# Kernel optimization log

Hardware: AMD Instinct MI355X
Metric: run time of the kernel (lower is better)

## Reference

```python
import jax, jax.numpy as jnp
import numpy as np

B, T, C = 2, 2048, 2048
N_HEAD, N_KV = 16, 4
HD = C // N_HEAD          # 128
ROPE_THETA = 10000.0


def setup_inputs() -> dict:
    key = jax.random.key(0)
    ks = jax.random.split(key, 6)
    std = 0.02
    x = jax.random.normal(ks[0], (B, T, C), dtype=jnp.float32)
    Wq = jax.random.normal(ks[1], (C, C), dtype=jnp.float32) * std
    Wk = jax.random.normal(ks[2], (C, N_KV * HD), dtype=jnp.float32) * std
    Wv = jax.random.normal(ks[3], (C, N_KV * HD), dtype=jnp.float32) * std
    Wo = jax.random.normal(ks[4], (C, C), dtype=jnp.float32) * std
    # real RoPE frequencies: freqs_cis = exp(i * t * theta^{-2j/hd})
    inv_freq = 1.0 / (ROPE_THETA ** (jnp.arange(0, HD, 2, dtype=jnp.float32) / HD))
    ang = jnp.arange(T, dtype=jnp.float32)[:, None] * inv_freq[None, :]  # [T, HD//2]
    return {"x": x, "Wq": Wq, "Wk": Wk, "Wv": Wv, "Wo": Wo,
            "freqs_cos": jnp.cos(ang), "freqs_sin": jnp.sin(ang)}


def _rope(t, cos, sin):
    # t: [B, H, T, HD]; cos/sin: [T, HD//2] -> complex rotate even/odd pairs
    tr = t.reshape(*t.shape[:-1], HD // 2, 2)
    re, im = tr[..., 0], tr[..., 1]
    c = cos[None, None, :, :]
    s = sin[None, None, :, :]
    out = jnp.stack([re * c - im * s, re * s + im * c], axis=-1)
    return out.reshape(t.shape)


def reference(x, Wq, Wk, Wv, Wo, freqs_cos, freqs_sin):
    Bm, Tm, Cm = x.shape
    q = (x @ Wq).reshape(Bm, Tm, N_HEAD, HD).transpose(0, 2, 1, 3)  # [B,H,T,HD]
    k = (x @ Wk).reshape(Bm, Tm, N_KV, HD).transpose(0, 2, 1, 3)    # [B,Hkv,T,HD]
    v = (x @ Wv).reshape(Bm, Tm, N_KV, HD).transpose(0, 2, 1, 3)
    q = _rope(q, freqs_cos, freqs_sin)
    k = _rope(k, freqs_cos, freqs_sin)
    rep = N_HEAD // N_KV
    k = jnp.repeat(k, rep, axis=1)  # GQA repeat_kv -> [B,H,T,HD]
    v = jnp.repeat(v, rep, axis=1)
    scale = 1.0 / jnp.sqrt(jnp.asarray(HD, dtype=x.dtype))
    att = jnp.einsum("bhqd,bhkd->bhqk", q, k) * scale
    causal = jnp.tril(jnp.ones((Tm, Tm), dtype=bool))
    att = jnp.where(causal[None, None], att, jnp.asarray(-jnp.inf, att.dtype))
    att = jax.nn.softmax(att, axis=-1)
    y = jnp.einsum("bhqk,bhkd->bhqd", att, v)
    y = y.transpose(0, 2, 1, 3).reshape(Bm, Tm, Cm)
    return y @ Wo
```

## Files before the change

### kernel.cpp

```cpp
#include <hip/hip_runtime.h>

#define B_ 2
#define T_ 2048
#define C_ 2048
#define NH_ 16
#define NKV_ 4
#define HD_ 128
#define REP_ (NH_ / NKV_)
#define LDQKV 3072

typedef unsigned short u16;
typedef __bf16 bf16x8v __attribute__((ext_vector_type(8)));
typedef float f32x4v __attribute__((ext_vector_type(4)));

__device__ __forceinline__ u16 f2bf(float f) {
    unsigned int u;
    __builtin_memcpy(&u, &f, 4);
    u += 0x7FFFu + ((u >> 16) & 1u);
    return (u16)(u >> 16);
}
__device__ __forceinline__ unsigned int cvtpk(float a, float b) {
    unsigned int r;
    asm("v_cvt_pk_bf16_f32 %0, %1, %2" : "=v"(r) : "v"(a), "v"(b));
    return r;
}
__device__ __forceinline__ bf16x8v load8(const u16* p) {
    return *reinterpret_cast<const bf16x8v*>(p);
}
__device__ __forceinline__ void gl16(const u16* g, u16* l) {
    __builtin_amdgcn_global_load_lds(
        (const __attribute__((address_space(1))) void*)(g),
        (__attribute__((address_space(3))) void*)(l), 16, 0, 0);
}
__device__ __forceinline__ void stg(const u16* g, u16* l, int tid, int K) {
    gl16(g, l + tid * 8);
    gl16(g + (size_t)64 * K, l + 4096 + tid * 8);
}
__device__ __forceinline__ void stgB3(const u16* g, u16* l, int tid, int K) {
    gl16(g, l + tid * 8);
    gl16(g + (size_t)64 * K, l + 4096 + tid * 8);
    gl16(g + (size_t)128 * K, l + 8192 + tid * 8);
}
#define BAR()      __builtin_amdgcn_s_barrier()
#define LGKM0()    asm volatile("s_waitcnt lgkmcnt(0)" ::: "memory")
#define SCHED0()   __builtin_amdgcn_sched_barrier(0)
#define PRIO(x)    __builtin_amdgcn_s_setprio(x)

__global__ void cvt_f32_bf16(const float* __restrict__ in, u16* __restrict__ out, int n4) {
    int i = blockIdx.x * blockDim.x + threadIdx.x;
    if (i >= n4) return;
    float4 v = reinterpret_cast<const float4*>(in)[i];
    ushort4 o;
    o.x = f2bf(v.x); o.y = f2bf(v.y); o.z = f2bf(v.z); o.w = f2bf(v.w);
    reinterpret_cast<ushort4*>(out)[i] = o;
}

__global__ void xpose_f32_bf16(const float* __restrict__ in, u16* __restrict__ out,
                               int R, int Cc) {
    __shared__ u16 tile[32][33];
    int bx = blockIdx.x * 32, by = blockIdx.y * 32;
    int tx = threadIdx.x, ty = threadIdx.y;
    for (int i = 0; i < 32; i += 8)
        tile[ty + i][tx] = f2bf(in[(size_t)(by + ty + i) * Cc + bx + tx]);
    __syncthreads();
    for (int i = 0; i < 32; i += 8)
        out[(size_t)(bx + ty + i) * R + by + tx] = tile[tx][ty + i];
}

__global__ __launch_bounds__(512, 2) void gemm_qkv(const u16* __restrict__ A,
                                                   const u16* __restrict__ BT,
                                                   u16* __restrict__ Cq,
                                                   u16* __restrict__ vtb,
                                                   const float* __restrict__ cb,
                                                   const float* __restrict__ sb,
                                                   int M, int N, int K) {
    __shared__ __align__(16) u16 As[2][2][8192];
    __shared__ __align__(16) u16 Bs[2][12288];
    int tid = threadIdx.x;
    int lane = tid & 63, wave = tid >> 6;
    int wm = wave >> 2, wn = wave & 3;
    int m15 = lane & 15, quad = lane >> 4;

    int nbx = N / 192;
    int bid = blockIdx.x, cpx = gridDim.x >> 3;
    int swz = (bid & 7) * cpx + (bid >> 3);
    int m0 = (swz / nbx) * 256, n0 = (swz % nbx) * 192;

    int r_ = tid >> 3, c_ = tid & 7;
    const u16* gA0 = A + (size_t)(m0 + r_) * K + ((c_ ^ (r_ & 7)) * 8);
    const u16* gB0 = BT + (size_t)(n0 + r_) * K + ((c_ ^ (r_ & 7)) * 8);

    int sw8 = m15 & 7;
    int co0 = (quad ^ sw8) * 8;
    int co1 = ((4 + quad) ^ sw8) * 8;
    const u16* aB = &As[0][0][0] + wm * 8192 + m15 * 64;
    const u16* bB = &Bs[0][0] + (wn * 48 + m15) * 64;

    f32x4v acc[8][3] = {};
    int NT = K >> 6;

    stgB3(gB0, &Bs[0][0], tid, K);
    stg(gA0, &As[0][0][0], tid, K);
    stg(gA0 + (size_t)128 * K, &As[0][1][0], tid, K);
    stgB3(gB0 + 64, &Bs[1][0], tid, K);
    asm volatile("s_waitcnt vmcnt(3)" ::: "memory");
    SCHED0();
    BAR();

    for (int t = 0; t < NT; t++) {
        int d = t & 1;
        const u16* aT = aB + d * 16384;
        const u16* bT = bB + d * 12288;
        bf16x8v a0[4][2], a1[4][2], bv[3][2];

#pragma unroll
        for (int mt = 0; mt < 4; mt++) {
            a0[mt][0] = load8(aT + mt * 1024 + co0);
            a0[mt][1] = load8(aT + mt * 1024 + co1);
        }
#pragma unroll
        for (int nt = 0; nt < 2; nt++) {
            bv[nt][0] = load8(bT + nt * 1024 + co0);
            bv[nt][1] = load8(bT + nt * 1024 + co1);
        }
        if (t + 1 < NT) stg(gA0 + (t + 1) * 64, &As[1 - d][0][0], tid, K);
        BAR(); LGKM0(); SCHED0(); PRIO(1);
#pragma unroll
        for (int kc = 0; kc < 2; kc++)
#pragma unroll
            for (int mt = 0; mt < 4; mt++)
#pragma unroll
                for (int nt = 0; nt < 2; nt++)
                    acc[mt][nt] = __builtin_amdgcn_mfma_f32_16x16x32_bf16(
                        a0[mt][kc], bv[nt][kc], acc[mt][nt], 0, 0, 0);
        PRIO(0); BAR();

#pragma unroll
        for (int mt = 0; mt < 4; mt++) {
            a1[mt][0] = load8(aT + (mt + 4) * 1024 + co0);
            a1[mt][1] = load8(aT + (mt + 4) * 1024 + co1);
        }
        bv[2][0] = load8(bT + 2048 + co0);
        bv[2][1] = load8(bT + 2048 + co1);
        if (t + 1 < NT) stg(gA0 + (size_t)128 * K + (t + 1) * 64, &As[1 - d][1][0], tid, K);
        BAR(); LGKM0(); SCHED0(); PRIO(1);
#pragma unroll
        for (int kc = 0; kc < 2; kc++)
#pragma unroll
            for (int mt = 0; mt < 4; mt++)
#pragma unroll
                for (int nt = 0; nt < 2; nt++)
                    acc[mt + 4][nt] = __builtin_amdgcn_mfma_f32_16x16x32_bf16(
                        a1[mt][kc], bv[nt][kc], acc[mt + 4][nt], 0, 0, 0);
        PRIO(0); BAR();

        if (t + 2 < NT) stgB3(gB0 + (t + 2) * 64, &Bs[d][0], tid, K);
        PRIO(1);
#pragma unroll
        for (int kc = 0; kc < 2; kc++)
#pragma unroll
            for (int mt = 0; mt < 4; mt++)
                acc[mt][2] = __builtin_amdgcn_mfma_f32_16x16x32_bf16(
                    a0[mt][kc], bv[2][kc], acc[mt][2], 0, 0, 0);
#pragma unroll
        for (int kc = 0; kc < 2; kc++)
#pragma unroll
            for (int mt = 0; mt < 4; mt++)
                acc[mt + 4][2] = __builtin_amdgcn_mfma_f32_16x16x32_bf16(
                    a1[mt][kc], bv[2][kc], acc[mt + 4][2], 0, 0, 0);
        PRIO(0);
        if (t + 2 < NT) { asm volatile("s_waitcnt vmcnt(3)" ::: "memory"); }
        else            { asm volatile("s_waitcnt vmcnt(0)" ::: "memory"); }
        SCHED0();
        BAR();
    }

#pragma unroll
    for (int mt = 0; mt < 8; mt++)
#pragma unroll
        for (int nt = 0; nt < 3; nt++) {
            int c = n0 + wn * 48 + nt * 16 + m15;
            if (c >= 2560) {
                int hd = c - 2560;
                int mbase = m0 + wm * 128 + mt * 16 + quad * 4;
                int bb = mbase >> 11, tok = mbase & 2047;
                int g = (tok & 31) >> 2;
                int off = (tok & ~31) + ((g & 3) * 8 + (g >> 2) * 4);
                ushort4 pk;
                pk.x = f2bf(acc[mt][nt][0]);
                pk.y = f2bf(acc[mt][nt][1]);
                pk.z = f2bf(acc[mt][nt][2]);
                pk.w = f2bf(acc[mt][nt][3]);
                *reinterpret_cast<ushort4*>(vtb + ((size_t)bb * 512 + hd) * T_ + off) = pk;
            } else {
                int i = (c & 127) >> 1;
                float sgn = (c & 1) ? 1.f : -1.f;
#pragma unroll
                for (int r = 0; r < 4; r++) {
                    int mrow = m0 + wm * 128 + mt * 16 + quad * 4 + r;
                    int tok = mrow & 2047;
                    float cv = cb[tok * 64 + i];
                    float sv = sb[tok * 64 + i];
                    float v = acc[mt][nt][r];
                    float pval = __shfl_xor(v, 1, 64);
                    float outv = fmaf(v, cv, pval * sv * sgn);
                    Cq[(size_t)mrow * N + c] = f2bf(outv);
                }
            }
        }
}

__global__ __launch_bounds__(512, 2) void gemm_out(const u16* __restrict__ A,
                                                   const u16* __restrict__ BT,
                                                   float* __restrict__ C,
                                                   int M, int N, int K) {
    __shared__ __align__(16) u16 As2[2][8192];
    __shared__ __align__(16) u16 Bs2[2][2][8192];
    int tid = threadIdx.x;
    int lane = tid & 63, wave = tid >> 6;
    int wm = wave >> 2, wn = wave & 3;
    int m15 = lane & 15, quad = lane >> 4;

    int nbx = N >> 8;
    int bid = blockIdx.x, cpx = gridDim.x >> 3;
    int swz = (bid & 7) * cpx + (bid >> 3);
    int m0 = (swz / nbx) * 128, n0 = (swz % nbx) * 256;

    const u16* gA0 = A + (size_t)(m0 + (tid >> 3)) * K + (((tid & 7) ^ ((tid >> 3) & 7)) * 8);
    const u16* gB0 = BT + (size_t)(n0 + (tid >> 3)) * K + (((tid & 7) ^ ((tid >> 3) & 7)) * 8);

    int sw8 = m15 & 7;
    int co0 = (quad ^ sw8) * 8;
    int co1 = ((4 + quad) ^ sw8) * 8;
    const u16* aB = &As2[0][0] + (wm * 64 + m15) * 64;
    const u16* bB = &Bs2[0][0][0] + (wn >> 1) * 8192 + ((wn & 1) * 64 + m15) * 64;

    f32x4v acc[4][4] = {};
    int NT = K >> 6;

    stg(gB0, &Bs2[0][0][0], tid, K);
    stg(gB0 + (size_t)128 * K, &Bs2[0][1][0], tid, K);
    stg(gA0, &As2[0][0], tid, K);
    stg(gB0 + 64, &Bs2[1][0][0], tid, K);
    stg(gB0 + (size_t)128 * K + 64, &Bs2[1][1][0], tid, K);
    asm volatile("s_waitcnt vmcnt(4)" ::: "memory");
    SCHED0();
    BAR();

    for (int t = 0; t < NT; t++) {
        int d = t & 1;
        const u16* aT = aB + d * 8192;
        const u16* bT = bB + d * 16384;
        bf16x8v a0[2][2], a1[2][2], b0[2][2], b1[2][2];

#pragma unroll
        for (int mt = 0; mt < 2; mt++) {
            a0[mt][0] = load8(aT + mt * 1024 + co0);
            a0[mt][1] = load8(aT + mt * 1024 + co1);
        }
#pragma unroll
        for (int nt = 0; nt < 2; nt++) {
            b0[nt][0] = load8(bT + nt * 1024 + co0);
            b0[nt][1] = load8(bT + nt * 1024 + co1);
        }
        if (t + 1 < NT) stg(gA0 + (t + 1) * 64, &As2[1 - d][0], tid, K);
        BAR(); LGKM0(); SCHED0(); PRIO(1);
#pragma unroll
        for (int kc = 0; kc < 2; kc++)
#pragma unroll
            for (int mt = 0; mt < 2; mt++)
#pragma unroll
                for (int nt = 0; nt < 2; nt++)
                    acc[mt][nt] = __builtin_amdgcn_mfma_f32_16x16x32_bf16(
                        a0[mt][kc], b0[nt][kc], acc[mt][nt], 0, 0, 0);
        PRIO(0); BAR();

#pragma unroll
        for (int nt = 0; nt < 2; nt++) {
            b1[nt][0] = load8(bT + (nt + 2) * 1024 + co0);
            b1[nt][1] = load8(bT + (nt + 2) * 1024 + co1);
        }
        BAR(); LGKM0(); SCHED0(); PRIO(1);
#pragma unroll
        for (int kc = 0; kc < 2; kc++)
#pragma unroll
            for (int mt = 0; mt < 2; mt++)
#pragma unroll
                for (int nt = 0; nt < 2; nt++)
                    acc[mt][nt + 2] = __builtin_amdgcn_mfma_f32_16x16x32_bf16(
                        a0[mt][kc], b1[nt][kc], acc[mt][nt + 2], 0, 0, 0);
        PRIO(0); BAR();

#pragma unroll
        for (int mt = 0; mt < 2; mt++) {
            a1[mt][0] = load8(aT + (mt + 2) * 1024 + co0);
            a1[mt][1] = load8(aT + (mt + 2) * 1024 + co1);
        }
        if (t + 2 < NT) stg(gB0 + (t + 2) * 64, &Bs2[d][0][0], tid, K);
        BAR(); LGKM0(); SCHED0(); PRIO(1);
#pragma unroll
        for (int kc = 0; kc < 2; kc++)
#pragma unroll
            for (int mt = 0; mt < 2; mt++)
#pragma unroll
                for (int nt = 0; nt < 2; nt++)
                    acc[mt + 2][nt] = __builtin_amdgcn_mfma_f32_16x16x32_bf16(
                        a1[mt][kc], b0[nt][kc], acc[mt + 2][nt], 0, 0, 0);
        PRIO(0); BAR();

        if (t + 2 < NT) stg(gB0 + (size_t)128 * K + (t + 2) * 64, &Bs2[d][1][0], tid, K);
        BAR(); PRIO(1);
#pragma unroll
        for (int kc = 0; kc < 2; kc++)
#pragma unroll
            for (int mt = 0; mt < 2; mt++)
#pragma unroll
                for (int nt = 0; nt < 2; nt++)
                    acc[mt + 2][nt + 2] = __builtin_amdgcn_mfma_f32_16x16x32_bf16(
                        a1[mt][kc], b1[nt][kc], acc[mt + 2][nt + 2], 0, 0, 0);
        PRIO(0);
        if (t + 2 < NT) { asm volatile("s_waitcnt vmcnt(4)" ::: "memory"); }
        else            { asm volatile("s_waitcnt vmcnt(0)" ::: "memory"); }
        SCHED0();
        BAR();
    }

#pragma unroll
    for (int mt = 0; mt < 4; mt++)
#pragma unroll
        for (int nt = 0; nt < 4; nt++) {
            int c = n0 + wn * 64 + nt * 16 + m15;
#pragma unroll
            for (int r = 0; r < 4; r++) {
                int mrow = m0 + wm * 64 + mt * 16 + quad * 4 + r;
                C[(size_t)mrow * N + c] = acc[mt][nt][r];
            }
        }
}

__device__ __forceinline__ void stgK64(const u16* kB, u16* Kl, int kt, int tid) {
    int keyc = tid >> 4, ch = tid & 15;
    const u16* g = kB + (size_t)(kt + keyc) * LDQKV + (ch ^ keyc) * 8;
    u16* l = Kl + tid * 8;
#pragma unroll
    for (int j = 0; j < 4; j++) {
        gl16(g, l);
        g += (size_t)16 * LDQKV;
        l += 2048;
    }
}
__device__ __forceinline__ void stgV64(const u16* vB, u16* Vl, int kt, int tid) {
    int hdc = tid >> 3, ch = tid & 7;
    const u16* g = vB + (size_t)hdc * T_ + kt + (ch ^ (hdc & 7)) * 8;
    u16* l = Vl + tid * 8;
#pragma unroll
    for (int j = 0; j < 4; j++) {
        gl16(g, l);
        g += (size_t)32 * T_;
        l += 2048;
    }
}

__global__ __launch_bounds__(256) void flash_k(const u16* __restrict__ qkv,
                                               const u16* __restrict__ vtb,
                                               u16* __restrict__ yb) {
    __shared__ __align__(16) u16 Kl[2][64 * 128];
    __shared__ __align__(16) u16 Vl[2][128 * 64];
    int h = blockIdx.y, b = blockIdx.z;
    int kv = h / REP_;
    int tid = threadIdx.x;
    int lane = tid & 63, wave = tid >> 6;
    int m15 = lane & 15, quad = lane >> 4;
    int sw8 = m15 & 7;
    const u16* kB = qkv + (size_t)b * T_ * LDQKV + 2048 + kv * HD_;
    const u16* vB = vtb + ((size_t)(b * NKV_ + kv)) * HD_ * T_;
    const float scale2 = 0.1275173723f;
    const float M0b = 8.0f;
    const float NEG = -3.0e38f;

    for (int p = 0; p < 2; p++) {
        int qt = (p == 0) ? (int)blockIdx.x : (31 - (int)blockIdx.x);
        int qt0 = qt * 64;
        int q_i = qt0 + wave * 16 + m15;
        const u16* qp = qkv + (size_t)(b * T_ + q_i) * LDQKV + h * HD_ + quad * 8;
        bf16x8v qf[4];
#pragma unroll
        for (int kc = 0; kc < 4; kc++) qf[kc] = load8(qp + kc * 32);
        f32x4v o[8] = {};
        f32x4v lacc = {};
        int NT = qt + 1;

        stgK64(kB, &Kl[0][0], 0, tid);
        stgV64(vB, &Vl[0][0], 0, tid);
        asm volatile("s_waitcnt vmcnt(0)" ::: "memory");
        SCHED0();
        BAR();

        for (int it = 0; it < NT; it++) {
            int cur = it & 1;
            int kt = it * 64;
            const u16* Kc = &Kl[cur][0];
            const u16* Vc = &Vl[cur][0];

            bf16x8v kf[4][4];
#pragma unroll
            for (int nt = 0; nt < 4; nt++) {
                const u16* kls = Kc + (nt * 16 + m15) * 128;
#pragma unroll
                for (int kc = 0; kc < 4; kc++)
                    kf[nt][kc] = load8(kls + (((kc * 4 + quad) ^ m15) * 8));
            }
            if (it + 1 < NT) {
                stgK64(kB, &Kl[1 - cur][0], kt + 64, tid);
                stgV64(vB, &Vl[1 - cur][0], kt + 64, tid);
            }
            SCHED0();
            f32x4v s4[4] = {};
            PRIO(1);
#pragma unroll
            for (int nt = 0; nt < 4; nt++)
#pragma unroll
                for (int kc = 0; kc < 4; kc++)
                    s4[nt] = __builtin_amdgcn_mfma_f32_16x16x32_bf16(
                        kf[nt][kc], qf[kc], s4[nt], 0, 0, 0);
            PRIO(0);
            bf16x8v vf[2][8];
#pragma unroll
            for (int c = 0; c < 2; c++)
#pragma unroll
                for (int dt = 0; dt < 8; dt++)
                    vf[c][dt] = load8(Vc + (dt * 16 + m15) * 64 + (((c * 4 + quad) ^ sw8) * 8));
            if (kt + 64 > qt0) {
#pragma unroll
                for (int nt = 0; nt < 4; nt++) {
                    int key = kt + nt * 16 + quad * 4;
#pragma unroll
                    for (int r = 0; r < 4; r++)
                        if (key + r > q_i) s4[nt][r] = NEG;
                }
            }
#pragma unroll
            for (int nt = 0; nt < 4; nt++) {
#pragma unroll
                for (int r = 0; r < 4; r++)
                    s4[nt][r] = exp2f(fmaf(s4[nt][r], scale2, -M0b));
                lacc += s4[nt];
            }
            bf16x8v pf[2];
#pragma unroll
            for (int c = 0; c < 2; c++) {
                unsigned int w[4];
                w[0] = cvtpk(s4[2 * c][0], s4[2 * c][1]);
                w[1] = cvtpk(s4[2 * c][2], s4[2 * c][3]);
                w[2] = cvtpk(s4[2 * c + 1][0], s4[2 * c + 1][1]);
                w[3] = cvtpk(s4[2 * c + 1][2], s4[2 * c + 1][3]);
                __builtin_memcpy(&pf[c], w, 16);
            }
            PRIO(1);
#pragma unroll
            for (int c = 0; c < 2; c++)
#pragma unroll
                for (int dt = 0; dt < 8; dt++)
                    o[dt] = __builtin_amdgcn_mfma_f32_16x16x32_bf16(
                        vf[c][dt], pf[c], o[dt], 0, 0, 0);
            PRIO(0);
            if (it + 1 < NT) { asm volatile("s_waitcnt vmcnt(0)" ::: "memory"); }
            SCHED0();
            BAR();
        }

        float l = lacc[0] + lacc[1] + lacc[2] + lacc[3];
        l += __shfl_xor(l, 16, 64);
        l += __shfl_xor(l, 32, 64);
        float inv = 1.f / l;
        u16* yp = yb + (size_t)(b * T_ + q_i) * C_ + h * HD_ + quad * 4;
#pragma unroll
        for (int dt = 0; dt < 8; dt++) {
            ushort4 pk;
            pk.x = f2bf(o[dt][0] * inv);
            pk.y = f2bf(o[dt][1] * inv);
            pk.z = f2bf(o[dt][2] * inv);
            pk.w = f2bf(o[dt][3] * inv);
            *reinterpret_cast<ushort4*>(yp + dt * 16) = pk;
        }
    }
}

extern "C" void kernel_launch(void* const* d_in, const int* in_sizes, int n_in,
                              void* d_out, int out_size, void* d_ws, size_t ws_size,
                              hipStream_t stream) {
    const float* x  = (const float*)d_in[0];
    const float* Wq = (const float*)d_in[1];
    const float* Wk = (const float*)d_in[2];
    const float* Wv = (const float*)d_in[3];
    const float* Wo = (const float*)d_in[4];
    const float* fc = (const float*)d_in[5];
    const float* fs = (const float*)d_in[6];
    float* out = (float*)d_out;

    char* ws = (char*)d_ws;
    u16* WqkvT = (u16*)(ws);
    u16* WoT   = (u16*)(ws + 12582912);
    u16* xb    = (u16*)(ws + 20971520);
    u16* qkvb  = (u16*)(ws + 37748736);
    u16* vtb   = (u16*)(ws + 62914560);
    u16* yb    = (u16*)(ws + 67108864);

    const int M = B_ * T_;

    int n4 = (M * C_) / 4;
    cvt_f32_bf16<<<n4 / 256, 256, 0, stream>>>(x, xb, n4);

    dim3 tb(32, 8);
    xpose_f32_bf16<<<dim3(C_ / 32, C_ / 32), tb, 0, stream>>>(Wq, WqkvT, C_, C_);
    xpose_f32_bf16<<<dim3((NKV_ * HD_) / 32, C_ / 32), tb, 0, stream>>>(Wk, WqkvT + 2048 * 2048, C_, NKV_ * HD_);
    xpose_f32_bf16<<<dim3((NKV_ * HD_) / 32, C_ / 32), tb, 0, stream>>>(Wv, WqkvT + 2560 * 2048, C_, NKV_ * HD_);
    xpose_f32_bf16<<<dim3(C_ / 32, C_ / 32), tb, 0, stream>>>(Wo, WoT, C_, C_);

    gemm_qkv<<<dim3((LDQKV / 192) * (M / 256)), 512, 0, stream>>>(xb, WqkvT, qkvb, vtb, fc, fs, M, LDQKV, C_);

    flash_k<<<dim3(T_ / 128, NH_, B_), 256, 0, stream>>>(qkvb, vtb, yb);

    gemm_out<<<dim3((C_ / 256) * (M / 128)), 512, 0, stream>>>(yb, WoT, out, M, C_, C_);
}
```

Before: 288.6 us.

## Fuse prep kernels and process paired query tiles jointly in flash attention

The five conversion and transpose launches are merged into one prep kernel that dispatches on block index, which removes launch overhead and small-grid tails. The flash kernel now processes its two query tiles (the low and the mirrored high tile) in a single pass over the K/V stream, so each K/V tile is loaded into LDS once and reused for both query sets instead of being streamed twice. This roughly doubles accumulator register pressure (two output sets, two score sets), which may lower occupancy or cause spills.

```diff
diff --git a/kernel.cpp b/kernel.cpp
--- a/kernel.cpp
+++ b/kernel.cpp
@@ -46,20 +46,30 @@
 #define SCHED0()   __builtin_amdgcn_sched_barrier(0)
 #define PRIO(x)    __builtin_amdgcn_s_setprio(x)
 
-__global__ void cvt_f32_bf16(const float* __restrict__ in, u16* __restrict__ out, int n4) {
-    int i = blockIdx.x * blockDim.x + threadIdx.x;
-    if (i >= n4) return;
-    float4 v = reinterpret_cast<const float4*>(in)[i];
-    ushort4 o;
-    o.x = f2bf(v.x); o.y = f2bf(v.y); o.z = f2bf(v.z); o.w = f2bf(v.w);
-    reinterpret_cast<ushort4*>(out)[i] = o;
-}
-
-__global__ void xpose_f32_bf16(const float* __restrict__ in, u16* __restrict__ out,
-                               int R, int Cc) {
+__global__ void prep(const float* __restrict__ x,
+                     const float* __restrict__ Wq, const float* __restrict__ Wk,
+                     const float* __restrict__ Wv, const float* __restrict__ Wo,
+                     u16* __restrict__ xb, u16* __restrict__ WqkvT,
+                     u16* __restrict__ WoT) {
     __shared__ u16 tile[32][33];
-    int bx = blockIdx.x * 32, by = blockIdx.y * 32;
-    int tx = threadIdx.x, ty = threadIdx.y;
+    int bid = blockIdx.x, tid = threadIdx.x;
+    if (bid < 8192) {
+        int i = bid * 256 + tid;
+        float4 v = reinterpret_cast<const float4*>(x)[i];
+        ushort4 o;
+        o.x = f2bf(v.x); o.y = f2bf(v.y); o.z = f2bf(v.z); o.w = f2bf(v.w);
+        reinterpret_cast<ushort4*>(xb)[i] = o;
+        return;
+    }
+    int r = bid - 8192;
+    const float* in; u16* out; int Cc, nbx;
+    if (r < 4096)      { in = Wq; out = WqkvT;               Cc = 2048; nbx = 64; }
+    else if (r < 5120) { in = Wk; out = WqkvT + 2048 * 2048; Cc = 512;  nbx = 16; r -= 4096; }
+    else if (r < 6144) { in = Wv; out = WqkvT + 2560 * 2048; Cc = 512;  nbx = 16; r -= 5120; }
+    else               { in = Wo; out = WoT;                 Cc = 2048; nbx = 64; r -= 6144; }
+    int bx = (r % nbx) * 32, by = (r / nbx) * 32;
+    int tx = tid & 31, ty = tid >> 5;
+    const int R = 2048;
     for (int i = 0; i < 32; i += 8)
         tile[ty + i][tx] = f2bf(in[(size_t)(by + ty + i) * Cc + bx + tx]);
     __syncthreads();
@@ -378,109 +388,168 @@
     const float M0b = 8.0f;
     const float NEG = -3.0e38f;
 
-    for (int p = 0; p < 2; p++) {
-        int qt = (p == 0) ? (int)blockIdx.x : (31 - (int)blockIdx.x);
-        int qt0 = qt * 64;
-        int q_i = qt0 + wave * 16 + m15;
-        const u16* qp = qkv + (size_t)(b * T_ + q_i) * LDQKV + h * HD_ + quad * 8;
-        bf16x8v qf[4];
-#pragma unroll
-        for (int kc = 0; kc < 4; kc++) qf[kc] = load8(qp + kc * 32);
-        f32x4v o[8] = {};
-        f32x4v lacc = {};
-        int NT = qt + 1;
-
-        stgK64(kB, &Kl[0][0], 0, tid);
-        stgV64(vB, &Vl[0][0], 0, tid);
-        asm volatile("s_waitcnt vmcnt(0)" ::: "memory");
+    int xa = blockIdx.x;
+    int qa0 = xa * 64, qb0 = (31 - xa) * 64;
+    int NTa = xa + 1, NT = 32 - xa;
+    int q_ia = qa0 + wave * 16 + m15;
+    int q_ib = qb0 + wave * 16 + m15;
+    const u16* qpA = qkv + (size_t)(b * T_ + q_ia) * LDQKV + h * HD_ + quad * 8;
+    const u16* qpB = qkv + (size_t)(b * T_ + q_ib) * LDQKV + h * HD_ + quad * 8;
+    bf16x8v qfA[4], qfB[4];
+#pragma unroll
+    for (int kc = 0; kc < 4; kc++) {
+        qfA[kc] = load8(qpA + kc * 32);
+        qfB[kc] = load8(qpB + kc * 32);
+    }
+    f32x4v oA[8] = {}, oB[8] = {};
+    f32x4v laccA = {}, laccB = {};
+
+    stgK64(kB, &Kl[0][0], 0, tid);
+    stgV64(vB, &Vl[0][0], 0, tid);
+    asm volatile("s_waitcnt vmcnt(0)" ::: "memory");
+    SCHED0();
+    BAR();
+
+    for (int it = 0; it < NT; it++) {
+        int cur = it & 1;
+        int kt = it * 64;
+        const u16* Kc = &Kl[cur][0];
+        const u16* Vc = &Vl[cur][0];
+        bool actA = (it < NTa);
+
+        if (it + 1 < NT) {
+            stgK64(kB, &Kl[1 - cur][0], kt + 64, tid);
+            stgV64(vB, &Vl[1 - cur][0], kt + 64, tid);
+        }
+        SCHED0();
+
+        f32x4v sA[4] = {}, sB[4] = {};
+        PRIO(1);
+#pragma unroll
+        for (int nt = 0; nt < 4; nt++) {
+            const u16* kls = Kc + (nt * 16 + m15) * 128;
+            bf16x8v kf[4];
+#pragma unroll
+            for (int kc = 0; kc < 4; kc++)
+                kf[kc] = load8(kls + (((kc * 4 + quad) ^ m15) * 8));
+#pragma unroll
+            for (int kc = 0; kc < 4; kc++)
+                sB[nt] = __builtin_amdgcn_mfma_f32_16x16x32_bf16(
+                    kf[kc], qfB[kc], sB[nt], 0, 0, 0);
+            if (actA)
+#pragma unroll
+                for (int kc = 0; kc < 4; kc++)
+                    sA[nt] = __builtin_amdgcn_mfma_f32_16x16x32_bf16(
+                        kf[kc], qfA[kc], sA[nt], 0, 0, 0);
+        }
+        PRIO(0);
+
+        if (kt + 64 > qb0) {
+#pragma unroll
+            for (int nt = 0; nt < 4; nt++) {
+                int key = kt + nt * 16 + quad * 4;
+#pragma unroll
+                for (int r = 0; r < 4; r++)
+                    if (key + r > q_ib) sB[nt][r] = NEG;
+            }
+        }
+#pragma unroll
+        for (int nt = 0; nt < 4; nt++) {
+#pragma unroll
+            for (int r = 0; r < 4; r++)
+                sB[nt][r] = exp2f(fmaf(sB[nt][r], scale2, -M0b));
+            laccB += sB[nt];
+        }
+        bf16x8v pfA[2], pfB[2];
+#pragma unroll
+        for (int c = 0; c < 2; c++) {
+            unsigned int w[4];
+            w[0] = cvtpk(sB[2 * c][0], sB[2 * c][1]);
+            w[1] = cvtpk(sB[2 * c][2], sB[2 * c][3]);
+            w[2] = cvtpk(sB[2 * c + 1][0], sB[2 * c + 1][1]);
+            w[3] = cvtpk(sB[2 * c + 1][2], sB[2 * c + 1][3]);
+            __builtin_memcpy(&pfB[c], w, 16);
+        }
+        if (actA) {
+            if (kt + 64 > qa0) {
+#pragma unroll
+                for (int nt = 0; nt < 4; nt++) {
+                    int key = kt + nt * 16 + quad * 4;
+#pragma unroll
+                    for (int r = 0; r < 4; r++)
+                        if (key + r > q_ia) sA[nt][r] = NEG;
+                }
+            }
+#pragma unroll
+            for (int nt = 0; nt < 4; nt++) {
+#pragma unroll
+                for (int r = 0; r < 4; r++)
+                    sA[nt][r] = exp2f(fmaf(sA[nt][r], scale2, -M0b));
+                laccA += sA[nt];
+            }
+#pragma unroll
+            for (int c = 0; c < 2; c++) {
+                unsigned int w[4];
+                w[0] = cvtpk(sA[2 * c][0], sA[2 * c][1]);
+                w[1] = cvtpk(sA[2 * c][2], sA[2 * c][3]);
+                w[2] = cvtpk(sA[2 * c + 1][0], sA[2 * c + 1][1]);
+                w[3] = cvtpk(sA[2 * c + 1][2], sA[2 * c + 1][3]);
+                __builtin_memcpy(&pfA[c], w, 16);
+            }
+        }
+
+        PRIO(1);
+#pragma unroll
+        for (int c = 0; c < 2; c++) {
+            bf16x8v vf[8];
+#pragma unroll
+            for (int dt = 0; dt < 8; dt++)
+                vf[dt] = load8(Vc + (dt * 16 + m15) * 64 + (((c * 4 + quad) ^ sw8) * 8));
+#pragma unroll
+            for (int dt = 0; dt < 8; dt++)
+                oB[dt] = __builtin_amdgcn_mfma_f32_16x16x32_bf16(
+                    vf[dt], pfB[c], oB[dt], 0, 0, 0);
+            if (actA)
+#pragma unroll
+                for (int dt = 0; dt < 8; dt++)
+                    oA[dt] = __builtin_amdgcn_mfma_f32_16x16x32_bf16(
+                        vf[dt], pfA[c], oA[dt], 0, 0, 0);
+        }
+        PRIO(0);
+        if (it + 1 < NT) { asm volatile("s_waitcnt vmcnt(0)" ::: "memory"); }
         SCHED0();
         BAR();
-
-        for (int it = 0; it < NT; it++) {
-            int cur = it & 1;
-            int kt = it * 64;
-            const u16* Kc = &Kl[cur][0];
-            const u16* Vc = &Vl[cur][0];
-
-            bf16x8v kf[4][4];
-#pragma unroll
-            for (int nt = 0; nt < 4; nt++) {
-                const u16* kls = Kc + (nt * 16 + m15) * 128;
-#pragma unroll
-                for (int kc = 0; kc < 4; kc++)
-                    kf[nt][kc] = load8(kls + (((kc * 4 + quad) ^ m15) * 8));
-            }
-            if (it + 1 < NT) {
-                stgK64(kB, &Kl[1 - cur][0], kt + 64, tid);
-                stgV64(vB, &Vl[1 - cur][0], kt + 64, tid);
-            }
-            SCHED0();
-            f32x4v s4[4] = {};
-            PRIO(1);
-#pragma unroll
-            for (int nt = 0; nt < 4; nt++)
-#pragma unroll
-                for (int kc = 0; kc < 4; kc++)
-                    s4[nt] = __builtin_amdgcn_mfma_f32_16x16x32_bf16(
-                        kf[nt][kc], qf[kc], s4[nt], 0, 0, 0);
-            PRIO(0);
-            bf16x8v vf[2][8];
-#pragma unroll
-            for (int c = 0; c < 2; c++)
-#pragma unroll
-                for (int dt = 0; dt < 8; dt++)
-                    vf[c][dt] = load8(Vc + (dt * 16 + m15) * 64 + (((c * 4 + quad) ^ sw8) * 8));
-            if (kt + 64 > qt0) {
-#pragma unroll
-                for (int nt = 0; nt < 4; nt++) {
-                    int key = kt + nt * 16 + quad * 4;
-#pragma unroll
-                    for (int r = 0; r < 4; r++)
-                        if (key + r > q_i) s4[nt][r] = NEG;
-                }
-            }
-#pragma unroll
-            for (int nt = 0; nt < 4; nt++) {
-#pragma unroll
-                for (int r = 0; r < 4; r++)
-                    s4[nt][r] = exp2f(fmaf(s4[nt][r], scale2, -M0b));
-                lacc += s4[nt];
-            }
-            bf16x8v pf[2];
-#pragma unroll
-            for (int c = 0; c < 2; c++) {
-                unsigned int w[4];
-                w[0] = cvtpk(s4[2 * c][0], s4[2 * c][1]);
-                w[1] = cvtpk(s4[2 * c][2], s4[2 * c][3]);
-                w[2] = cvtpk(s4[2 * c + 1][0], s4[2 * c + 1][1]);
-                w[3] = cvtpk(s4[2 * c + 1][2], s4[2 * c + 1][3]);
-                __builtin_memcpy(&pf[c], w, 16);
-            }
-            PRIO(1);
-#pragma unroll
-            for (int c = 0; c < 2; c++)
-#pragma unroll
-                for (int dt = 0; dt < 8; dt++)
-                    o[dt] = __builtin_amdgcn_mfma_f32_16x16x32_bf16(
-                        vf[c][dt], pf[c], o[dt], 0, 0, 0);
-            PRIO(0);
-            if (it + 1 < NT) { asm volatile("s_waitcnt vmcnt(0)" ::: "memory"); }
-            SCHED0();
-            BAR();
-        }
-
-        float l = lacc[0] + lacc[1] + lacc[2] + lacc[3];
+    }
+
+    {
+        float l = laccA[0] + laccA[1] + laccA[2] + laccA[3];
         l += __shfl_xor(l, 16, 64);
         l += __shfl_xor(l, 32, 64);
         float inv = 1.f / l;
-        u16* yp = yb + (size_t)(b * T_ + q_i) * C_ + h * HD_ + quad * 4;
+        u16* yp = yb + (size_t)(b * T_ + q_ia) * C_ + h * HD_ + quad * 4;
 #pragma unroll
         for (int dt = 0; dt < 8; dt++) {
             ushort4 pk;
-            pk.x = f2bf(o[dt][0] * inv);
-            pk.y = f2bf(o[dt][1] * inv);
-            pk.z = f2bf(o[dt][2] * inv);
-            pk.w = f2bf(o[dt][3] * inv);
+            pk.x = f2bf(oA[dt][0] * inv);
+            pk.y = f2bf(oA[dt][1] * inv);
+            pk.z = f2bf(oA[dt][2] * inv);
+            pk.w = f2bf(oA[dt][3] * inv);
+            *reinterpret_cast<ushort4*>(yp + dt * 16) = pk;
+        }
+    }
+    {
+        float l = laccB[0] + laccB[1] + laccB[2] + laccB[3];
+        l += __shfl_xor(l, 16, 64);
+        l += __shfl_xor(l, 32, 64);
+        float inv = 1.f / l;
+        u16* yp = yb + (size_t)(b * T_ + q_ib) * C_ + h * HD_ + quad * 4;
+#pragma unroll
+        for (int dt = 0; dt < 8; dt++) {
+            ushort4 pk;
+            pk.x = f2bf(oB[dt][0] * inv);
+            pk.y = f2bf(oB[dt][1] * inv);
+            pk.z = f2bf(oB[dt][2] * inv);
+            pk.w = f2bf(oB[dt][3] * inv);
             *reinterpret_cast<ushort4*>(yp + dt * 16) = pk;
         }
     }
@@ -508,14 +577,7 @@
 
     const int M = B_ * T_;
 
-    int n4 = (M * C_) / 4;
-    cvt_f32_bf16<<<n4 / 256, 256, 0, stream>>>(x, xb, n4);
-
-    dim3 tb(32, 8);
-    xpose_f32_bf16<<<dim3(C_ / 32, C_ / 32), tb, 0, stream>>>(Wq, WqkvT, C_, C_);
-    xpose_f32_bf16<<<dim3((NKV_ * HD_) / 32, C_ / 32), tb, 0, stream>>>(Wk, WqkvT + 2048 * 2048, C_, NKV_ * HD_);
-    xpose_f32_bf16<<<dim3((NKV_ * HD_) / 32, C_ / 32), tb, 0, stream>>>(Wv, WqkvT + 2560 * 2048, C_, NKV_ * HD_);
-    xpose_f32_bf16<<<dim3(C_ / 32, C_ / 32), tb, 0, stream>>>(Wo, WoT, C_, C_);
+    prep<<<dim3(18432), 256, 0, stream>>>(x, Wq, Wk, Wv, Wo, xb, WqkvT, WoT);
 
     gemm_qkv<<<dim3((LDQKV / 192) * (M / 256)), 512, 0, stream>>>(xb, WqkvT, qkvb, vtb, fc, fs, M, LDQKV, C_);
 
```

Result: slower. 341.5 us (+18.3%).

## Merge prep kernels into one launch and remap flash blocks for KV locality

Applied to the files above, without the earlier changes.

The x conversion and the four weight-transpose launches are merged into a single prep kernel that dispatches on block index, which removes four launches and lets all the work fill the GPU together. The flash attention grid is flattened and remapped so that consecutive blocks (bid & 7) span all eight (batch, kv-group) combinations, while the heads sharing one KV group are spread across blocks 128 apart. The intent is to spread work across XCDs (blocks are typically dispatched round-robin across the 8 XCDs on this chip) so that each XCD serves a single (batch, kv-group) and gets better L2 reuse of K/V. The risk is a different load balance or dispatch order for the causal tiles.

```diff
diff --git a/kernel.cpp b/kernel.cpp
--- a/kernel.cpp
+++ b/kernel.cpp
@@ -46,20 +46,30 @@
 #define SCHED0()   __builtin_amdgcn_sched_barrier(0)
 #define PRIO(x)    __builtin_amdgcn_s_setprio(x)
 
-__global__ void cvt_f32_bf16(const float* __restrict__ in, u16* __restrict__ out, int n4) {
-    int i = blockIdx.x * blockDim.x + threadIdx.x;
-    if (i >= n4) return;
-    float4 v = reinterpret_cast<const float4*>(in)[i];
-    ushort4 o;
-    o.x = f2bf(v.x); o.y = f2bf(v.y); o.z = f2bf(v.z); o.w = f2bf(v.w);
-    reinterpret_cast<ushort4*>(out)[i] = o;
-}
-
-__global__ void xpose_f32_bf16(const float* __restrict__ in, u16* __restrict__ out,
-                               int R, int Cc) {
+__global__ void prep(const float* __restrict__ x,
+                     const float* __restrict__ Wq, const float* __restrict__ Wk,
+                     const float* __restrict__ Wv, const float* __restrict__ Wo,
+                     u16* __restrict__ xb, u16* __restrict__ WqkvT,
+                     u16* __restrict__ WoT) {
     __shared__ u16 tile[32][33];
-    int bx = blockIdx.x * 32, by = blockIdx.y * 32;
-    int tx = threadIdx.x, ty = threadIdx.y;
+    int bid = blockIdx.x, tid = threadIdx.x;
+    if (bid < 8192) {
+        int i = bid * 256 + tid;
+        float4 v = reinterpret_cast<const float4*>(x)[i];
+        ushort4 o;
+        o.x = f2bf(v.x); o.y = f2bf(v.y); o.z = f2bf(v.z); o.w = f2bf(v.w);
+        reinterpret_cast<ushort4*>(xb)[i] = o;
+        return;
+    }
+    int r = bid - 8192;
+    const float* in; u16* out; int Cc, nbx;
+    if (r < 4096)      { in = Wq; out = WqkvT;               Cc = 2048; nbx = 64; }
+    else if (r < 5120) { in = Wk; out = WqkvT + 2048 * 2048; Cc = 512;  nbx = 16; r -= 4096; }
+    else if (r < 6144) { in = Wv; out = WqkvT + 2560 * 2048; Cc = 512;  nbx = 16; r -= 5120; }
+    else               { in = Wo; out = WoT;                 Cc = 2048; nbx = 64; r -= 6144; }
+    int bx = (r % nbx) * 32, by = (r / nbx) * 32;
+    int tx = tid & 31, ty = tid >> 5;
+    const int R = 2048;
     for (int i = 0; i < 32; i += 8)
         tile[ty + i][tx] = f2bf(in[(size_t)(by + ty + i) * Cc + bx + tx]);
     __syncthreads();
@@ -366,8 +376,12 @@
                                                u16* __restrict__ yb) {
     __shared__ __align__(16) u16 Kl[2][64 * 128];
     __shared__ __align__(16) u16 Vl[2][128 * 64];
-    int h = blockIdx.y, b = blockIdx.z;
-    int kv = h / REP_;
+    int bid = blockIdx.x;
+    int grp = bid & 7;
+    int b = grp >> 2, kv = grp & 3;
+    int rr = bid >> 3;
+    int xa = rr & 15;
+    int h = kv * REP_ + (rr >> 4);
     int tid = threadIdx.x;
     int lane = tid & 63, wave = tid >> 6;
     int m15 = lane & 15, quad = lane >> 4;
@@ -379,7 +393,7 @@
     const float NEG = -3.0e38f;
 
     for (int p = 0; p < 2; p++) {
-        int qt = (p == 0) ? (int)blockIdx.x : (31 - (int)blockIdx.x);
+        int qt = (p == 0) ? xa : (31 - xa);
         int qt0 = qt * 64;
         int q_i = qt0 + wave * 16 + m15;
         const u16* qp = qkv + (size_t)(b * T_ + q_i) * LDQKV + h * HD_ + quad * 8;
@@ -508,18 +522,11 @@
 
     const int M = B_ * T_;
 
-    int n4 = (M * C_) / 4;
-    cvt_f32_bf16<<<n4 / 256, 256, 0, stream>>>(x, xb, n4);
-
-    dim3 tb(32, 8);
-    xpose_f32_bf16<<<dim3(C_ / 32, C_ / 32), tb, 0, stream>>>(Wq, WqkvT, C_, C_);
-    xpose_f32_bf16<<<dim3((NKV_ * HD_) / 32, C_ / 32), tb, 0, stream>>>(Wk, WqkvT + 2048 * 2048, C_, NKV_ * HD_);
-    xpose_f32_bf16<<<dim3((NKV_ * HD_) / 32, C_ / 32), tb, 0, stream>>>(Wv, WqkvT + 2560 * 2048, C_, NKV_ * HD_);
-    xpose_f32_bf16<<<dim3(C_ / 32, C_ / 32), tb, 0, stream>>>(Wo, WoT, C_, C_);
+    prep<<<dim3(18432), 256, 0, stream>>>(x, Wq, Wk, Wv, Wo, xb, WqkvT, WoT);
 
     gemm_qkv<<<dim3((LDQKV / 192) * (M / 256)), 512, 0, stream>>>(xb, WqkvT, qkvb, vtb, fc, fs, M, LDQKV, C_);
 
-    flash_k<<<dim3(T_ / 128, NH_, B_), 256, 0, stream>>>(qkvb, vtb, yb);
+    flash_k<<<dim3(512), 256, 0, stream>>>(qkvb, vtb, yb);
 
     gemm_out<<<dim3((C_ / 256) * (M / 128)), 512, 0, stream>>>(yb, WoT, out, M, C_, C_);
 }
```

Measured after the change: 277.3 us. 3.9% less time.
